# Performance work log

Hardware: AMD Instinct MI355X
Metric: run time of the kernel (lower is better)

## Reference

```python
import jax, jax.numpy as jnp
import numpy as np

B, N, K = 32, 4096, 8          # batch, num input features (64x64 map), num slots
HID, D, DM = 256, 256, 512     # hid_dim, slot_dim, mlp_hid_dim
ITERS = 3
TEMP = 1.0
EPS = 1e-8
SCALE = D ** -0.5              # (slot_dim // num_heads) ** -0.5, heads=1


def layer_norm(x, g, b):
    m = jnp.mean(x, axis=-1, keepdims=True)
    v = jnp.mean((x - m) ** 2, axis=-1, keepdims=True)
    return (x - m) * jax.lax.rsqrt(v + 1e-5) * g + b


def setup_inputs() -> dict:
    key = jax.random.key(0)
    ks = jax.random.split(key, 20)
    s = 0.02
    inp = {
        "inputs": jax.random.normal(ks[0], (B, N, HID), jnp.float32),
        "noise": jax.random.normal(ks[1], (B, K, D), jnp.float32),
        "slots_mu": jax.random.normal(ks[2], (1, 1, D), jnp.float32),
        "slots_sigma": jnp.abs(jax.random.normal(ks[3], (1, 1, D), jnp.float32)),
        "ln_in_g": jnp.ones((HID,), jnp.float32),
        "ln_in_b": jnp.zeros((HID,), jnp.float32),
        "ln_slots_g": jnp.ones((D,), jnp.float32),
        "ln_slots_b": jnp.zeros((D,), jnp.float32),
        "ln_mlp_g": jnp.ones((D,), jnp.float32),
        "ln_mlp_b": jnp.zeros((D,), jnp.float32),
        # Linear weights stored [in, out]
        "Wq": jax.random.normal(ks[4], (D, D), jnp.float32) * s,
        "bq": jnp.zeros((D,), jnp.float32),
        "Wk": jax.random.normal(ks[5], (HID, D), jnp.float32) * s,
        "bk": jnp.zeros((D,), jnp.float32),
        "Wv": jax.random.normal(ks[6], (HID, D), jnp.float32) * s,
        "bv": jnp.zeros((D,), jnp.float32),
        # GRUCell params (torch layout transposed to [in, 3D])
        "W_ih": jax.random.normal(ks[7], (D, 3 * D), jnp.float32) * s,
        "W_hh": jax.random.normal(ks[8], (D, 3 * D), jnp.float32) * s,
        "b_ih": jnp.zeros((3 * D,), jnp.float32),
        "b_hh": jnp.zeros((3 * D,), jnp.float32),
        # residual MLP
        "W1": jax.random.normal(ks[9], (D, DM), jnp.float32) * s,
        "b1": jnp.zeros((DM,), jnp.float32),
        "W2": jax.random.normal(ks[10], (DM, D), jnp.float32) * s,
        "b2": jnp.zeros((D,), jnp.float32),
    }
    return inp


def reference(inputs, noise, slots_mu, slots_sigma,
              ln_in_g, ln_in_b, ln_slots_g, ln_slots_b, ln_mlp_g, ln_mlp_b,
              Wq, bq, Wk, bk, Wv, bv,
              W_ih, W_hh, b_ih, b_hh,
              W1, b1, W2, b2):
    x = layer_norm(inputs, ln_in_g, ln_in_b)            # [B,N,HID]
    k = x @ Wk + bk                                     # [B,N,D]
    v = x @ Wv + bv                                     # [B,N,D]

    slots = slots_mu + slots_sigma * noise              # [B,K,D]

    for _ in range(ITERS):
        slots_prev = slots
        s = layer_norm(slots, ln_slots_g, ln_slots_b)
        q = s @ Wq + bq                                  # [B,K,D]
        dots = jnp.einsum('bkd,bnd->bkn', q, k) * SCALE / TEMP
        attn = jax.nn.softmax(dots, axis=1)              # inverted: over slot axis
        attn = attn + EPS
        attn = attn / jnp.sum(attn, axis=2, keepdims=True)  # weighted mean over keys
        updates = jnp.einsum('bkn,bnd->bkd', attn, v)    # [B,K,D]

        # GRUCell on flattened (B*K, D)
        xg = updates.reshape(-1, D)
        h = slots_prev.reshape(-1, D)
        gi = xg @ W_ih + b_ih
        gh = h @ W_hh + b_hh
        i_r, i_z, i_n = jnp.split(gi, 3, axis=-1)
        h_r, h_z, h_n = jnp.split(gh, 3, axis=-1)
        r = jax.nn.sigmoid(i_r + h_r)
        z = jax.nn.sigmoid(i_z + h_z)
        n = jnp.tanh(i_n + r * h_n)
        h = (1.0 - z) * n + z * h
        slots = h.reshape(B, K, D)

        # residual MLP
        m = layer_norm(slots, ln_mlp_g, ln_mlp_b)
        slots = slots + (jax.nn.relu(m @ W1 + b1) @ W2 + b2)

    return slots
```

## Files before the change

kernel.cpp:

```cpp
#include <hip/hip_runtime.h>
#include <hip/hip_bf16.h>

#define NB 32
#define NPOS 4096
#define NSLOT 8
#define HIDD 256
#define DDIM 256
#define SCALE_F 0.0625f
#define EPS_F 1e-8f
#define NCHUNK 32
#define CPOS 128
#define TPOS 32

typedef __attribute__((ext_vector_type(4))) float f32x4;
typedef __attribute__((ext_vector_type(8))) short s16x8;
typedef __attribute__((ext_vector_type(2))) unsigned int u32x2;
typedef _Float16 h16x2 __attribute__((ext_vector_type(2)));

__device__ __forceinline__ unsigned short f2bf(float f) {
    unsigned int x = __float_as_uint(f);
    x = (x + 0x7fffu + ((x >> 16) & 1u)) >> 16;
    return (unsigned short)x;
}
__device__ __forceinline__ unsigned short f2h(float f) {
    _Float16 h = (_Float16)f;
    return __builtin_bit_cast(unsigned short, h);
}
__device__ __forceinline__ h16x2 u2h(unsigned u) { return __builtin_bit_cast(h16x2, u); }
__device__ __forceinline__ h16x2 mkh(float a0, float a1) {
    h16x2 r; r[0] = (_Float16)a0; r[1] = (_Float16)a1; return r;
}
__device__ __forceinline__ void dot4(f32x4& acc, uint4 wv, h16x2 av) {
    acc[0] = __builtin_amdgcn_fdot2(av, u2h(wv.x), acc[0], false);
    acc[1] = __builtin_amdgcn_fdot2(av, u2h(wv.y), acc[1], false);
    acc[2] = __builtin_amdgcn_fdot2(av, u2h(wv.z), acc[2], false);
    acc[3] = __builtin_amdgcn_fdot2(av, u2h(wv.w), acc[3], false);
}
__device__ __forceinline__ unsigned packrowh(const float* __restrict__ W, int hp, int N, int c) {
    return (unsigned)f2h(W[(2*hp)*N + c]) | ((unsigned)f2h(W[(2*hp+1)*N + c]) << 16);
}

__device__ __forceinline__ void qk_tail(
        float v0, float v1, int b, int s0,
        const float* __restrict__ lng, const float* __restrict__ lnb,
        const float* __restrict__ Wq, const float* __restrict__ bq,
        const float* __restrict__ Wk, const float* __restrict__ bk,
        unsigned short* __restrict__ qkg, float* __restrict__ qbkg,
        float (*sh)[256], float (*red)[4]) {
    int c = threadIdx.x;
    float s_0 = v0, q_0 = v0 * v0, s_1 = v1, q_1 = v1 * v1;
    #pragma unroll
    for (int m = 32; m; m >>= 1) {
        s_0 += __shfl_xor(s_0, m); q_0 += __shfl_xor(q_0, m);
        s_1 += __shfl_xor(s_1, m); q_1 += __shfl_xor(q_1, m);
    }
    if ((c & 63) == 0) { int w = c >> 6; red[w][0]=s_0; red[w][1]=q_0; red[w][2]=s_1; red[w][3]=q_1; }
    __syncthreads();
    float S0 = red[0][0]+red[1][0]+red[2][0]+red[3][0];
    float Q0 = red[0][1]+red[1][1]+red[2][1]+red[3][1];
    float S1 = red[0][2]+red[1][2]+red[2][2]+red[3][2];
    float Q1 = red[0][3]+red[1][3]+red[2][3]+red[3][3];
    float m0 = S0 * 0.00390625f, r0 = rsqrtf(Q0 * 0.00390625f - m0*m0 + 1e-5f);
    float m1 = S1 * 0.00390625f, r1 = rsqrtf(Q1 * 0.00390625f - m1*m1 + 1e-5f);
    float gc = lng[c], bc = lnb[c];
    sh[0][c] = (v0 - m0) * r0 * gc + bc;
    sh[1][c] = (v1 - m1) * r1 * gc + bc;
    __syncthreads();
    float qa0 = bq[c], qa1 = qa0;
    for (int h = 0; h < 256; h += 4) {
        float w0 = Wq[(h+0)*256+c], w1 = Wq[(h+1)*256+c];
        float w2 = Wq[(h+2)*256+c], w3 = Wq[(h+3)*256+c];
        float4 x0 = *(const float4*)&sh[0][h], x1 = *(const float4*)&sh[1][h];
        qa0 += x0.x*w0 + x0.y*w1 + x0.z*w2 + x0.w*w3;
        qa1 += x1.x*w0 + x1.y*w1 + x1.z*w2 + x1.w*w3;
    }
    __syncthreads();
    sh[0][c] = qa0; sh[1][c] = qa1;
    float bkc = bk[c];
    float p0 = qa0 * bkc, p1 = qa1 * bkc;
    #pragma unroll
    for (int m = 32; m; m >>= 1) { p0 += __shfl_xor(p0, m); p1 += __shfl_xor(p1, m); }
    __syncthreads();
    if ((c & 63) == 0) { int w = c >> 6; red[w][0] = p0; red[w][1] = p1; }
    __syncthreads();
    if (c < 2) qbkg[b*8 + s0 + c] = SCALE_F * (red[0][c]+red[1][c]+red[2][c]+red[3][c]);
    float k0 = 0.f, k1 = 0.f;
    const float* wkr = Wk + (long)c * 256;
    for (int d = 0; d < 256; d += 4) {
        float4 wk4 = *(const float4*)&wkr[d];
        float4 x0 = *(const float4*)&sh[0][d], x1 = *(const float4*)&sh[1][d];
        k0 += x0.x*wk4.x + x0.y*wk4.y + x0.z*wk4.z + x0.w*wk4.w;
        k1 += x1.x*wk4.x + x1.y*wk4.y + x1.z*wk4.z + x1.w*wk4.w;
    }
    qkg[(b*8 + s0    )*256 + c] = f2bf(SCALE_F * k0);
    qkg[(b*8 + s0 + 1)*256 + c] = f2bf(SCALE_F * k1);
}

__global__ __launch_bounds__(256) void k_setup(
        const float* __restrict__ x, const float* __restrict__ lnig,
        const float* __restrict__ lnib, unsigned short* __restrict__ lnx,
        const float* __restrict__ Wq, const float* __restrict__ Wk,
        const float* __restrict__ Wv, const float* __restrict__ Wih,
        const float* __restrict__ Whh, const float* __restrict__ W1,
        const float* __restrict__ W2,
        unsigned* __restrict__ WqP, unsigned* __restrict__ WkTP,
        unsigned* __restrict__ WvP, unsigned* __restrict__ WihP,
        unsigned* __restrict__ WhhP, unsigned* __restrict__ W1P,
        unsigned* __restrict__ W2P,
        const float* __restrict__ noise, const float* __restrict__ mu,
        const float* __restrict__ sig, const float* __restrict__ lnsg,
        const float* __restrict__ lnsb, const float* __restrict__ bq,
        const float* __restrict__ bk, float* __restrict__ slots,
        unsigned short* __restrict__ qkg, float* __restrict__ qbkg) {
    __shared__ float sh[2][256];
    __shared__ float red[4][4];
    if (blockIdx.x < 8192) {
        int lane = threadIdx.x & 63;
        int wave = threadIdx.x >> 6;
        long row = (long)blockIdx.x * 4 + wave;
        const float4* xr = (const float4*)(x + row * 256);
        float4 v = xr[lane];
        float s = v.x + v.y + v.z + v.w;
        float sq = v.x * v.x + v.y * v.y + v.z * v.z + v.w * v.w;
        #pragma unroll
        for (int m = 32; m; m >>= 1) { s += __shfl_xor(s, m); sq += __shfl_xor(sq, m); }
        float mean = s * 0.00390625f;
        float rstd = rsqrtf(sq * 0.00390625f - mean * mean + 1e-5f);
        const float4 gg = ((const float4*)lnig)[lane];
        const float4 bb = ((const float4*)lnib)[lane];
        ushort4 o;
        o.x = f2bf((v.x - mean) * rstd * gg.x + bb.x);
        o.y = f2bf((v.y - mean) * rstd * gg.y + bb.y);
        o.z = f2bf((v.z - mean) * rstd * gg.z + bb.z);
        o.w = f2bf((v.w - mean) * rstd * gg.w + bb.w);
        ((ushort4*)(lnx + row * 256))[lane] = o;
        return;
    }
    if (blockIdx.x < 8576) {
        int i = (blockIdx.x - 8192) * 256 + threadIdx.x;
        if (i < 32768) {
            int hp = i >> 8, c = i & 255;
            WqP[i] = packrowh(Wq, hp, 256, c);
            WvP[i] = packrowh(Wv, hp, 256, c);
            WkTP[i] = (unsigned)f2h(Wk[c*256 + 2*hp]) | ((unsigned)f2h(Wk[c*256 + 2*hp + 1]) << 16);
        }
        if (i < 65536) {
            int hp1 = i >> 9, c1 = i & 511;
            W1P[i] = packrowh(W1, hp1, 512, c1);
            int hp2 = i >> 8, c2 = i & 255;
            W2P[i] = packrowh(W2, hp2, 256, c2);
        }
        if (i < 98304) {
            int hp = i / 768, c = i % 768;
            WihP[i] = packrowh(Wih, hp, 768, c);
            WhhP[i] = packrowh(Whh, hp, 768, c);
        }
        return;
    }
    {
        int bi = blockIdx.x - 8576;
        int b = bi >> 2, rp = bi & 3;
        int s0 = rp * 2, r0 = b * 8 + s0;
        int c = threadIdx.x;
        float v0 = mu[c] + sig[c] * noise[r0*256 + c];
        float v1 = mu[c] + sig[c] * noise[(r0+1)*256 + c];
        slots[r0*256 + c] = v0;
        slots[(r0+1)*256 + c] = v1;
        qk_tail(v0, v1, b, s0, lnsg, lnsb, Wq, bq, Wk, bk, qkg, qbkg, sh, red);
    }
}

__global__ __launch_bounds__(128) void k_stream(
        const unsigned short* __restrict__ lnx, const unsigned short* __restrict__ qk,
        const float* __restrict__ qbk, float* __restrict__ Upart,
        float* __restrict__ dpart) {
    __shared__ unsigned short xt[TPOS * 256];
    __shared__ float Ured[8 * 256];
    __shared__ float dred[8];
    int b = blockIdx.x >> 5, ch = blockIdx.x & 31;
    int t = threadIdx.x;
    int l = t & 63, w = t >> 6;
    for (int i = t; i < 2048; i += 128) Ured[i] = 0.f;
    if (t < 8) dred[t] = 0.f;
    int slot = l & 15, g = l >> 4;
    s16x8 qkf[8];
    float qbkv = 0.f;
    if (slot < 8) {
        const unsigned short* qrow = qk + (b*8 + slot) * 256;
        #pragma unroll
        for (int hk = 0; hk < 8; hk++)
            qkf[hk] = *(const s16x8*)(qrow + hk*32 + 8*g);
        qbkv = qbk[b*8 + slot];
    } else {
        #pragma unroll
        for (int hk = 0; hk < 8; hk++) qkf[hk] = (s16x8)0;
    }
    f32x4 uacc[16];
    #pragma unroll
    for (int i = 0; i < 16; i++) uacc[i] = (f32x4)0.f;
    float dreg = 0.f;
    int gbase = (b * NPOS + ch * CPOS) * 256;
    int pw = w * 16;
    __syncthreads();
    for (int tile = 0; tile < 4; tile++) {
        #pragma unroll
        for (int i = 0; i < 8; i++) {
            int c = t + 128 * i;
            int p = c >> 5, hc = c & 31;
            int4 v = *(const int4*)(lnx + gbase + (tile*TPOS + p)*256 + hc*8);
            *(int4*)&xt[p*256 + ((hc ^ (p & 15)) << 3)] = v;
        }
        __syncthreads();
        f32x4 acc = (f32x4)0.f;
        {
            int prow = pw + (l & 15);
            const unsigned short* xrow = &xt[prow * 256];
            int sw = prow & 15;
            #pragma unroll
            for (int hk = 0; hk < 8; hk++) {
                s16x8 a = *(const s16x8*)(xrow + (((hk*4 + g) ^ sw) << 3));
                acc = __builtin_amdgcn_mfma_f32_16x16x32_bf16(a, qkf[hk], acc, 0, 0, 0);
            }
        }
        float at[4];
        #pragma unroll
        for (int r = 0; r < 4; r++) {
            float v = acc[r] + qbkv;
            float m = v;
            m = fmaxf(m, __shfl_xor(m, 1));
            m = fmaxf(m, __shfl_xor(m, 2));
            m = fmaxf(m, __shfl_xor(m, 4));
            float e = __expf(v - m);
            float sum = e;
            sum += __shfl_xor(sum, 1);
            sum += __shfl_xor(sum, 2);
            sum += __shfl_xor(sum, 4);
            float a = e / sum;
            at[r] = a;
            dreg += a;
        }
        u32x2 a2;
        a2.x = (unsigned)f2bf(at[0]) | ((unsigned)f2bf(at[1]) << 16);
        a2.y = (unsigned)f2bf(at[2]) | ((unsigned)f2bf(at[3]) << 16);
        int p0 = pw + 4 * g;
        int hl = l & 7;
        #pragma unroll
        for (int hc = 0; hc < 16; hc++) {
            int hcol = hc * 2 + ((l & 15) >> 3);
            unsigned e0 = xt[(p0+0)*256 + ((hcol ^ ((p0+0) & 15)) << 3) + hl];
            unsigned e1 = xt[(p0+1)*256 + ((hcol ^ ((p0+1) & 15)) << 3) + hl];
            unsigned e2 = xt[(p0+2)*256 + ((hcol ^ ((p0+2) & 15)) << 3) + hl];
            unsigned e3 = xt[(p0+3)*256 + ((hcol ^ ((p0+3) & 15)) << 3) + hl];
            u32x2 b2;
            b2.x = e0 | (e1 << 16);
            b2.y = e2 | (e3 << 16);
            asm volatile("v_mfma_f32_16x16x16_bf16 %0, %1, %2, %0"
                         : "+v"(uacc[hc]) : "v"(a2), "v"(b2));
        }
        __syncthreads();
    }
    if (g < 2) {
        #pragma unroll
        for (int hc = 0; hc < 16; hc++) {
            int h = hc * 16 + (l & 15);
            #pragma unroll
            for (int r = 0; r < 4; r++)
                atomicAdd(&Ured[(4*g + r)*256 + h], uacc[hc][r]);
        }
    }
    dreg += __shfl_xor(dreg, 16);
    dreg += __shfl_xor(dreg, 32);
    if (slot < 8 && g == 0) atomicAdd(&dred[slot], dreg);
    __syncthreads();
    float* up = Upart + (long)(b * NCHUNK + ch) * 2048;
    for (int i = t; i < 2048; i += 128) up[i] = Ured[i];
    if (t < 8) dpart[(b * NCHUNK + ch) * 8 + t] = dred[t];
}

__device__ __forceinline__ float ln1024(float v, int c, const float* __restrict__ g,
                                        const float* __restrict__ b, float (*red)[2]) {
    float s1 = v, s2 = v * v;
    #pragma unroll
    for (int m = 32; m; m >>= 1) { s1 += __shfl_xor(s1, m); s2 += __shfl_xor(s2, m); }
    int w = threadIdx.x >> 6;
    if ((threadIdx.x & 63) == 0) { red[w][0] = s1; red[w][1] = s2; }
    __syncthreads();
    float S = 0.f, Q = 0.f;
    #pragma unroll
    for (int i = 0; i < 16; i++) { S += red[i][0]; Q += red[i][1]; }
    float mean = S * (1.f/1024.f);
    float rstd = rsqrtf(Q * (1.f/1024.f) - mean*mean + 1e-5f);
    __syncthreads();
    return (v - mean) * rstd * g[c] + b[c];
}

__global__ __launch_bounds__(1024) void k_post(
        const float* __restrict__ Upart, const float* __restrict__ dpart,
        const unsigned* __restrict__ WvP, const float* __restrict__ bv,
        const unsigned* __restrict__ WihP, const unsigned* __restrict__ WhhP,
        const float* __restrict__ bih, const float* __restrict__ bhh,
        const float* __restrict__ lnmg, const float* __restrict__ lnmb,
        const unsigned* __restrict__ W1P, const float* __restrict__ b1,
        const unsigned* __restrict__ W2P, const float* __restrict__ b2,
        const float* __restrict__ lnsg, const float* __restrict__ lnsb,
        const unsigned* __restrict__ WqP, const float* __restrict__ bq,
        const unsigned* __restrict__ WkTP, const float* __restrict__ bk,
        float* __restrict__ slots, unsigned short* __restrict__ qkg,
        float* __restrict__ qbkg, float* __restrict__ outp, int last) {
    __shared__ union {
        float PG[2][8][768];
        struct { float P16[16][256]; float H2[8][512]; } s;
    } sm;
    __shared__ float A[256], B[256], G2[2][768], H[512];
    __shared__ float red[16][2];
    __shared__ float scal[1];
    int r = blockIdx.x, b = r >> 3, s = r & 7;
    int t = threadIdx.x, c = t & 255, q = t >> 8;
    int cg = t & 63, kg16 = t >> 6;
    {
        float u = 0.f;
        const float* ub = Upart + (long)b * NCHUNK * 2048 + s * 256 + c;
        #pragma unroll
        for (int i = 0; i < 8; i++) u += ub[(q * 8 + i) * 2048];
        sm.s.P16[q][c] = u;
        if (q == 1) B[c] = slots[r * 256 + c];
        if (t < 32) {
            float dv = dpart[(b * NCHUNK + t) * 8 + s];
            #pragma unroll
            for (int m = 16; m; m >>= 1) dv += __shfl_xor(dv, m);
            if (t == 0) scal[0] = dv;
        }
    }
    __syncthreads();
    float dn = 1.f / (scal[0] + (float)NPOS * EPS_F);
    if (q == 0) A[c] = sm.s.P16[0][c] + sm.s.P16[1][c] + sm.s.P16[2][c] + sm.s.P16[3][c];
    __syncthreads();
    {
        f32x4 acc = (f32x4)0.f;
        const uint4* wp = (const uint4*)(WvP + kg16 * 8 * 256 + 4 * cg);
        #pragma unroll
        for (int i = 0; i < 8; i++) {
            uint4 wv = wp[i * 64];
            dot4(acc, wv, mkh(A[2*(kg16*8+i)], A[2*(kg16*8+i)+1]));
        }
        *(f32x4*)&sm.s.P16[kg16][4*cg] = acc;
    }
    __syncthreads();
    float updtmp;
    {
        float ss = 0.f;
        #pragma unroll
        for (int k = 0; k < 16; k++) ss += sm.s.P16[k][c];
        updtmp = ss * dn + bv[c];
    }
    __syncthreads();
    if (q == 0) A[c] = updtmp;
    __syncthreads();
    {
        int h = t >> 9;
        int kg = (t >> 6) & 7;
        const float* src = h ? B : A;
        const unsigned* W = h ? WhhP : WihP;
        f32x4 ar = (f32x4)0.f, az = (f32x4)0.f, an = (f32x4)0.f;
        #pragma unroll 4
        for (int i = 0; i < 16; i++) {
            int hp = kg * 16 + i;
            h16x2 av = mkh(src[2*hp], src[2*hp+1]);
            uint4 w0 = *(const uint4*)(W + hp*768 + 4*cg);
            uint4 w1 = *(const uint4*)(W + hp*768 + 256 + 4*cg);
            uint4 w2 = *(const uint4*)(W + hp*768 + 512 + 4*cg);
            dot4(ar, w0, av);
            dot4(az, w1, av);
            dot4(an, w2, av);
        }
        *(f32x4*)&sm.PG[h][kg][4*cg]       = ar;
        *(f32x4*)&sm.PG[h][kg][256 + 4*cg] = az;
        *(f32x4*)&sm.PG[h][kg][512 + 4*cg] = an;
    }
    __syncthreads();
    for (int idx = t; idx < 1536; idx += 1024) {
        int h = idx / 768, cc = idx - h * 768;
        float ss = 0.f;
        #pragma unroll
        for (int k = 0; k < 8; k++) ss += sm.PG[h][k][cc];
        G2[h][cc] = ss;
    }
    __syncthreads();
    float spc = B[c];
    float gir = bih[c]     + G2[0][c];
    float giz = bih[c+256] + G2[0][c+256];
    float gin = bih[c+512] + G2[0][c+512];
    float ghr = bhh[c]     + G2[1][c];
    float ghz = bhh[c+256] + G2[1][c+256];
    float ghn = bhh[c+512] + G2[1][c+512];
    float rg = 1.f/(1.f + __expf(-(gir+ghr)));
    float zg = 1.f/(1.f + __expf(-(giz+ghz)));
    float ng = tanhf(gin + rg*ghn);
    float hnew = (1.f - zg)*ng + zg*spc;
    float mmc = ln1024(hnew, c, lnmg, lnmb, red);
    if (q == 0) A[c] = mmc;
    __syncthreads();
    {
        int kg = t >> 7, cg1 = t & 127;
        f32x4 acc = (f32x4)0.f;
        const uint4* wp = (const uint4*)(W1P + kg * 16 * 512 + 4 * cg1);
        #pragma unroll 4
        for (int i = 0; i < 16; i++) {
            uint4 wv = wp[i * 128];
            dot4(acc, wv, mkh(A[2*(kg*16+i)], A[2*(kg*16+i)+1]));
        }
        *(f32x4*)&sm.s.H2[kg][4*cg1] = acc;
    }
    __syncthreads();
    if (t < 512) {
        float ss = b1[t];
        #pragma unroll
        for (int k = 0; k < 8; k++) ss += sm.s.H2[k][t];
        H[t] = fmaxf(ss, 0.f);
    }
    __syncthreads();
    {
        f32x4 acc = (f32x4)0.f;
        const uint4* wp = (const uint4*)(W2P + kg16 * 16 * 256 + 4 * cg);
        #pragma unroll 4
        for (int i = 0; i < 16; i++) {
            uint4 wv = wp[i * 64];
            dot4(acc, wv, mkh(H[2*(kg16*16+i)], H[2*(kg16*16+i)+1]));
        }
        *(f32x4*)&sm.s.P16[kg16][4*cg] = acc;
    }
    __syncthreads();
    float outc;
    {
        float ss = 0.f;
        #pragma unroll
        for (int k = 0; k < 16; k++) ss += sm.s.P16[k][c];
        outc = hnew + ss + b2[c];
    }
    if (t < 256) {
        slots[r*256 + c] = outc;
        if (last) outp[r*256 + c] = outc;
    }
    if (last) return;
    __syncthreads();
    float sc = ln1024(outc, c, lnsg, lnsb, red);
    if (q == 0) A[c] = sc;
    __syncthreads();
    {
        f32x4 acc = (f32x4)0.f;
        const uint4* wp = (const uint4*)(WqP + kg16 * 8 * 256 + 4 * cg);
        #pragma unroll
        for (int i = 0; i < 8; i++) {
            uint4 wv = wp[i * 64];
            dot4(acc, wv, mkh(A[2*(kg16*8+i)], A[2*(kg16*8+i)+1]));
        }
        *(f32x4*)&sm.s.P16[kg16][4*cg] = acc;
    }
    __syncthreads();
    float qc;
    {
        float ss = 0.f;
        #pragma unroll
        for (int k = 0; k < 16; k++) ss += sm.s.P16[k][c];
        qc = ss + bq[c];
    }
    {
        float v = qc * bk[c];
        #pragma unroll
        for (int m = 32; m; m >>= 1) v += __shfl_xor(v, m);
        int w = t >> 6;
        if ((t & 63) == 0) red[w][0] = v;
        __syncthreads();
        if (t == 0) {
            float S = 0.f;
            #pragma unroll
            for (int i = 0; i < 16; i++) S += red[i][0];
            qbkg[r] = SCALE_F * 0.25f * S;
        }
        __syncthreads();
    }
    if (q == 0) A[c] = qc;
    __syncthreads();
    {
        f32x4 acc = (f32x4)0.f;
        const uint4* wp = (const uint4*)(WkTP + kg16 * 8 * 256 + 4 * cg);
        #pragma unroll
        for (int i = 0; i < 8; i++) {
            uint4 wv = wp[i * 64];
            dot4(acc, wv, mkh(A[2*(kg16*8+i)], A[2*(kg16*8+i)+1]));
        }
        *(f32x4*)&sm.s.P16[kg16][4*cg] = acc;
    }
    __syncthreads();
    if (t < 256) {
        float ss = 0.f;
        #pragma unroll
        for (int k = 0; k < 16; k++) ss += sm.s.P16[k][c];
        qkg[r*256 + c] = f2bf(SCALE_F * ss);
    }
}

extern "C" void kernel_launch(void* const* d_in, const int* in_sizes, int n_in,
                              void* d_out, int out_size, void* d_ws, size_t ws_size,
                              hipStream_t stream) {
    const float* inputs = (const float*)d_in[0];
    const float* noise  = (const float*)d_in[1];
    const float* mu     = (const float*)d_in[2];
    const float* sig    = (const float*)d_in[3];
    const float* lnig   = (const float*)d_in[4];
    const float* lnib   = (const float*)d_in[5];
    const float* lnsg   = (const float*)d_in[6];
    const float* lnsb   = (const float*)d_in[7];
    const float* lnmg   = (const float*)d_in[8];
    const float* lnmb   = (const float*)d_in[9];
    const float* Wq     = (const float*)d_in[10];
    const float* bq     = (const float*)d_in[11];
    const float* Wk     = (const float*)d_in[12];
    const float* bk     = (const float*)d_in[13];
    const float* Wv     = (const float*)d_in[14];
    const float* bv     = (const float*)d_in[15];
    const float* Wih    = (const float*)d_in[16];
    const float* Whh    = (const float*)d_in[17];
    const float* bih    = (const float*)d_in[18];
    const float* bhh    = (const float*)d_in[19];
    const float* W1     = (const float*)d_in[20];
    const float* b1     = (const float*)d_in[21];
    const float* W2     = (const float*)d_in[22];
    const float* b2     = (const float*)d_in[23];

    char* ws = (char*)d_ws;
    unsigned short* lnx = (unsigned short*)ws;
    size_t off = (size_t)NB * NPOS * HIDD * 2;
    unsigned short* qkb = (unsigned short*)(ws + off); off += (size_t)NB*NSLOT*HIDD*2;
    float* qbk   = (float*)(ws + off); off += (size_t)NB*NSLOT*4;
    float* Upart = (float*)(ws + off); off += (size_t)NB*NCHUNK*NSLOT*HIDD*4;
    float* dpart = (float*)(ws + off); off += (size_t)NB*NCHUNK*NSLOT*4;
    float* slots = (float*)(ws + off); off += (size_t)NB*NSLOT*DDIM*4;
    unsigned* WqP  = (unsigned*)(ws + off); off += 32768u*4;
    unsigned* WkTP = (unsigned*)(ws + off); off += 32768u*4;
    unsigned* WvP  = (unsigned*)(ws + off); off += 32768u*4;
    unsigned* WihP = (unsigned*)(ws + off); off += 98304u*4;
    unsigned* WhhP = (unsigned*)(ws + off); off += 98304u*4;
    unsigned* W1P  = (unsigned*)(ws + off); off += 65536u*4;
    unsigned* W2P  = (unsigned*)(ws + off); off += 65536u*4;

    k_setup<<<8704, 256, 0, stream>>>(inputs, lnig, lnib, lnx,
                                      Wq, Wk, Wv, Wih, Whh, W1, W2,
                                      WqP, WkTP, WvP, WihP, WhhP, W1P, W2P,
                                      noise, mu, sig, lnsg, lnsb, bq, bk,
                                      slots, qkb, qbk);
    for (int it = 0; it < 3; it++) {
        k_stream<<<NB*NCHUNK, 128, 0, stream>>>(lnx, qkb, qbk, Upart, dpart);
        k_post<<<NB*NSLOT, 1024, 0, stream>>>(Upart, dpart,
                                              WvP, bv, WihP, WhhP, bih, bhh,
                                              lnmg, lnmb, W1P, b1, W2P, b2,
                                              lnsg, lnsb, WqP, bq, WkTP, bk,
                                              slots, qkb, qbk, (float*)d_out,
                                              it == 2 ? 1 : 0);
    }
}
```

Measured before the change: 216.1 us.

## Fuse stream and post kernels into one persistent kernel with grid barriers

Replaces the six alternating k_stream/k_post launches with a single persistent 256-block, 1024-thread kernel that runs all three iterations and synchronises through an atomic grid barrier in workspace. Each block now streams a 512-position region per batch in 16 tiles, with waves taking turns on the QK MFMA and attention written through shared memory. The goal is to remove launch overhead and gaps between kernels. In exchange the stream phase runs with fewer, larger blocks (256 instead of 1024), which lowers memory-level parallelism. The spin barrier also depends on all 256 blocks being co-resident.

```diff
diff --git a/kernel.cpp b/kernel.cpp
--- a/kernel.cpp
+++ b/kernel.cpp
@@ -4,13 +4,10 @@
 #define NB 32
 #define NPOS 4096
 #define NSLOT 8
-#define HIDD 256
-#define DDIM 256
 #define SCALE_F 0.0625f
 #define EPS_F 1e-8f
-#define NCHUNK 32
-#define CPOS 128
 #define TPOS 32
+#define NREG 8
 
 typedef __attribute__((ext_vector_type(4))) float f32x4;
 typedef __attribute__((ext_vector_type(8))) short s16x8;
@@ -38,6 +35,17 @@
 }
 __device__ __forceinline__ unsigned packrowh(const float* __restrict__ W, int hp, int N, int c) {
     return (unsigned)f2h(W[(2*hp)*N + c]) | ((unsigned)f2h(W[(2*hp+1)*N + c]) << 16);
+}
+
+__device__ __forceinline__ void gridbar(unsigned* cnt, unsigned target) {
+    __syncthreads();
+    if (threadIdx.x == 0) {
+        __threadfence();
+        __hip_atomic_fetch_add(cnt, 1u, __ATOMIC_RELEASE, __HIP_MEMORY_SCOPE_AGENT);
+        while (__hip_atomic_load(cnt, __ATOMIC_ACQUIRE, __HIP_MEMORY_SCOPE_AGENT) < target)
+            __builtin_amdgcn_s_sleep(8);
+    }
+    __syncthreads();
 }
 
 __device__ __forceinline__ void qk_tail(
@@ -111,7 +119,8 @@
         const float* __restrict__ sig, const float* __restrict__ lnsg,
         const float* __restrict__ lnsb, const float* __restrict__ bq,
         const float* __restrict__ bk, float* __restrict__ slots,
-        unsigned short* __restrict__ qkg, float* __restrict__ qbkg) {
+        unsigned short* __restrict__ qkg, float* __restrict__ qbkg,
+        unsigned* __restrict__ barcnt) {
     __shared__ float sh[2][256];
     __shared__ float red[4][4];
     if (blockIdx.x < 8192) {
@@ -137,6 +146,7 @@
         return;
     }
     if (blockIdx.x < 8576) {
+        if (blockIdx.x == 8192 && threadIdx.x == 0) *barcnt = 0u;
         int i = (blockIdx.x - 8192) * 256 + threadIdx.x;
         if (i < 32768) {
             int hp = i >> 8, c = i & 255;
@@ -170,132 +180,26 @@
     }
 }
 
-__global__ __launch_bounds__(128) void k_stream(
-        const unsigned short* __restrict__ lnx, const unsigned short* __restrict__ qk,
-        const float* __restrict__ qbk, float* __restrict__ Upart,
-        float* __restrict__ dpart) {
-    __shared__ unsigned short xt[TPOS * 256];
-    __shared__ float Ured[8 * 256];
-    __shared__ float dred[8];
-    int b = blockIdx.x >> 5, ch = blockIdx.x & 31;
-    int t = threadIdx.x;
-    int l = t & 63, w = t >> 6;
-    for (int i = t; i < 2048; i += 128) Ured[i] = 0.f;
-    if (t < 8) dred[t] = 0.f;
-    int slot = l & 15, g = l >> 4;
-    s16x8 qkf[8];
-    float qbkv = 0.f;
-    if (slot < 8) {
-        const unsigned short* qrow = qk + (b*8 + slot) * 256;
-        #pragma unroll
-        for (int hk = 0; hk < 8; hk++)
-            qkf[hk] = *(const s16x8*)(qrow + hk*32 + 8*g);
-        qbkv = qbk[b*8 + slot];
-    } else {
-        #pragma unroll
-        for (int hk = 0; hk < 8; hk++) qkf[hk] = (s16x8)0;
-    }
-    f32x4 uacc[16];
-    #pragma unroll
-    for (int i = 0; i < 16; i++) uacc[i] = (f32x4)0.f;
-    float dreg = 0.f;
-    int gbase = (b * NPOS + ch * CPOS) * 256;
-    int pw = w * 16;
-    __syncthreads();
-    for (int tile = 0; tile < 4; tile++) {
-        #pragma unroll
-        for (int i = 0; i < 8; i++) {
-            int c = t + 128 * i;
-            int p = c >> 5, hc = c & 31;
-            int4 v = *(const int4*)(lnx + gbase + (tile*TPOS + p)*256 + hc*8);
-            *(int4*)&xt[p*256 + ((hc ^ (p & 15)) << 3)] = v;
-        }
-        __syncthreads();
-        f32x4 acc = (f32x4)0.f;
-        {
-            int prow = pw + (l & 15);
-            const unsigned short* xrow = &xt[prow * 256];
-            int sw = prow & 15;
-            #pragma unroll
-            for (int hk = 0; hk < 8; hk++) {
-                s16x8 a = *(const s16x8*)(xrow + (((hk*4 + g) ^ sw) << 3));
-                acc = __builtin_amdgcn_mfma_f32_16x16x32_bf16(a, qkf[hk], acc, 0, 0, 0);
-            }
-        }
-        float at[4];
-        #pragma unroll
-        for (int r = 0; r < 4; r++) {
-            float v = acc[r] + qbkv;
-            float m = v;
-            m = fmaxf(m, __shfl_xor(m, 1));
-            m = fmaxf(m, __shfl_xor(m, 2));
-            m = fmaxf(m, __shfl_xor(m, 4));
-            float e = __expf(v - m);
-            float sum = e;
-            sum += __shfl_xor(sum, 1);
-            sum += __shfl_xor(sum, 2);
-            sum += __shfl_xor(sum, 4);
-            float a = e / sum;
-            at[r] = a;
-            dreg += a;
-        }
-        u32x2 a2;
-        a2.x = (unsigned)f2bf(at[0]) | ((unsigned)f2bf(at[1]) << 16);
-        a2.y = (unsigned)f2bf(at[2]) | ((unsigned)f2bf(at[3]) << 16);
-        int p0 = pw + 4 * g;
-        int hl = l & 7;
-        #pragma unroll
-        for (int hc = 0; hc < 16; hc++) {
-            int hcol = hc * 2 + ((l & 15) >> 3);
-            unsigned e0 = xt[(p0+0)*256 + ((hcol ^ ((p0+0) & 15)) << 3) + hl];
-            unsigned e1 = xt[(p0+1)*256 + ((hcol ^ ((p0+1) & 15)) << 3) + hl];
-            unsigned e2 = xt[(p0+2)*256 + ((hcol ^ ((p0+2) & 15)) << 3) + hl];
-            unsigned e3 = xt[(p0+3)*256 + ((hcol ^ ((p0+3) & 15)) << 3) + hl];
-            u32x2 b2;
-            b2.x = e0 | (e1 << 16);
-            b2.y = e2 | (e3 << 16);
-            asm volatile("v_mfma_f32_16x16x16_bf16 %0, %1, %2, %0"
-                         : "+v"(uacc[hc]) : "v"(a2), "v"(b2));
-        }
-        __syncthreads();
-    }
-    if (g < 2) {
-        #pragma unroll
-        for (int hc = 0; hc < 16; hc++) {
-            int h = hc * 16 + (l & 15);
-            #pragma unroll
-            for (int r = 0; r < 4; r++)
-                atomicAdd(&Ured[(4*g + r)*256 + h], uacc[hc][r]);
-        }
-    }
-    dreg += __shfl_xor(dreg, 16);
-    dreg += __shfl_xor(dreg, 32);
-    if (slot < 8 && g == 0) atomicAdd(&dred[slot], dreg);
-    __syncthreads();
-    float* up = Upart + (long)(b * NCHUNK + ch) * 2048;
-    for (int i = t; i < 2048; i += 128) up[i] = Ured[i];
-    if (t < 8) dpart[(b * NCHUNK + ch) * 8 + t] = dred[t];
-}
-
-__device__ __forceinline__ float ln1024(float v, int c, const float* __restrict__ g,
-                                        const float* __restrict__ b, float (*red)[2]) {
-    float s1 = v, s2 = v * v;
-    #pragma unroll
-    for (int m = 32; m; m >>= 1) { s1 += __shfl_xor(s1, m); s2 += __shfl_xor(s2, m); }
-    int w = threadIdx.x >> 6;
-    if ((threadIdx.x & 63) == 0) { red[w][0] = s1; red[w][1] = s2; }
-    __syncthreads();
-    float S = 0.f, Q = 0.f;
-    #pragma unroll
-    for (int i = 0; i < 16; i++) { S += red[i][0]; Q += red[i][1]; }
-    float mean = S * (1.f/1024.f);
-    float rstd = rsqrtf(Q * (1.f/1024.f) - mean*mean + 1e-5f);
-    __syncthreads();
-    return (v - mean) * rstd * g[c] + b[c];
-}
-
-__global__ __launch_bounds__(1024) void k_post(
-        const float* __restrict__ Upart, const float* __restrict__ dpart,
+struct StreamS {
+    unsigned short xt[TPOS * 256];
+    float Ured[8 * 256];
+    float attnL[32][9];
+    float dred[8];
+};
+struct PostS {
+    union {
+        float PG[2][8][768];
+        struct { float P16[16][256]; float H2[8][512]; } s;
+    } sm;
+    float A[256], B[256], G2[2][768], H[512];
+    float red[16][2];
+    float scal[1];
+};
+
+__global__ __launch_bounds__(1024) void k_loop(
+        const unsigned short* __restrict__ lnx,
+        unsigned short* __restrict__ qkg, float* __restrict__ qbkg,
+        float* __restrict__ Upart, float* __restrict__ dpart,
         const unsigned* __restrict__ WvP, const float* __restrict__ bv,
         const unsigned* __restrict__ WihP, const unsigned* __restrict__ WhhP,
         const float* __restrict__ bih, const float* __restrict__ bhh,
@@ -305,198 +209,329 @@
         const float* __restrict__ lnsg, const float* __restrict__ lnsb,
         const unsigned* __restrict__ WqP, const float* __restrict__ bq,
         const unsigned* __restrict__ WkTP, const float* __restrict__ bk,
-        float* __restrict__ slots, unsigned short* __restrict__ qkg,
-        float* __restrict__ qbkg, float* __restrict__ outp, int last) {
-    __shared__ union {
-        float PG[2][8][768];
-        struct { float P16[16][256]; float H2[8][512]; } s;
-    } sm;
-    __shared__ float A[256], B[256], G2[2][768], H[512];
-    __shared__ float red[16][2];
-    __shared__ float scal[1];
-    int r = blockIdx.x, b = r >> 3, s = r & 7;
-    int t = threadIdx.x, c = t & 255, q = t >> 8;
-    int cg = t & 63, kg16 = t >> 6;
-    {
-        float u = 0.f;
-        const float* ub = Upart + (long)b * NCHUNK * 2048 + s * 256 + c;
-        #pragma unroll
-        for (int i = 0; i < 8; i++) u += ub[(q * 8 + i) * 2048];
-        sm.s.P16[q][c] = u;
-        if (q == 1) B[c] = slots[r * 256 + c];
-        if (t < 32) {
-            float dv = dpart[(b * NCHUNK + t) * 8 + s];
-            #pragma unroll
-            for (int m = 16; m; m >>= 1) dv += __shfl_xor(dv, m);
-            if (t == 0) scal[0] = dv;
+        float* __restrict__ slots, float* __restrict__ outp,
+        unsigned* __restrict__ barcnt) {
+    __shared__ union { StreamS st; PostS po; } smem;
+    int blk = blockIdx.x;
+    int t = threadIdx.x;
+    int l = t & 63, w = t >> 6;
+    int bS = blk >> 3, region = blk & 7;
+    int rP = blk, bP = blk >> 3, sP = blk & 7;
+    unsigned barno = 0;
+    for (int it = 0; it < 3; it++) {
+        {
+            StreamS& S = smem.st;
+            for (int i = t; i < 2048; i += 1024) S.Ured[i] = 0.f;
+            if (t < 8) S.dred[t] = 0.f;
+            int slot = l & 15, g = l >> 4;
+            s16x8 qkf[8];
+            float qbkv = 0.f;
+            if (slot < 8) {
+                const unsigned short* qrow = qkg + (bS*8 + slot) * 256;
+                #pragma unroll
+                for (int hk = 0; hk < 8; hk++)
+                    qkf[hk] = *(const s16x8*)(qrow + hk*32 + 8*g);
+                qbkv = qbkg[bS*8 + slot];
+            } else {
+                #pragma unroll
+                for (int hk = 0; hk < 8; hk++) qkf[hk] = (s16x8)0;
+            }
+            f32x4 uacc = (f32x4)0.f;
+            float dreg = 0.f;
+            long gbase = ((long)bS * NPOS + region * 512) * 256;
+            int pw = (w & 1) * 16;
+            __syncthreads();
+            for (int tile = 0; tile < 16; tile++) {
+                {
+                    int p = t >> 5, hc = t & 31;
+                    int4 v = *((const int4*)(lnx + gbase + tile*(32*256)) + t);
+                    *(int4*)&S.xt[p*256 + ((hc ^ (p & 15)) << 3)] = v;
+                }
+                __syncthreads();
+                if ((w >> 1) == (tile & 7)) {
+                    f32x4 acc = (f32x4)0.f;
+                    int prow = pw + slot;
+                    const unsigned short* xrow = &S.xt[prow * 256];
+                    int sw = prow & 15;
+                    #pragma unroll
+                    for (int hk = 0; hk < 8; hk++) {
+                        s16x8 a = *(const s16x8*)(xrow + (((hk*4 + g) ^ sw) << 3));
+                        acc = __builtin_amdgcn_mfma_f32_16x16x32_bf16(a, qkf[hk], acc, 0, 0, 0);
+                    }
+                    #pragma unroll
+                    for (int r = 0; r < 4; r++) {
+                        float v = acc[r] + qbkv;
+                        float m = v;
+                        m = fmaxf(m, __shfl_xor(m, 1));
+                        m = fmaxf(m, __shfl_xor(m, 2));
+                        m = fmaxf(m, __shfl_xor(m, 4));
+                        float e = __expf(v - m);
+                        float sum = e;
+                        sum += __shfl_xor(sum, 1);
+                        sum += __shfl_xor(sum, 2);
+                        sum += __shfl_xor(sum, 4);
+                        float a = e / sum;
+                        if (slot < 8) { S.attnL[pw + 4*g + r][slot] = a; dreg += a; }
+                    }
+                }
+                __syncthreads();
+                {
+                    int hl = l & 7;
+                    int hcol = w * 2 + (slot >> 3);
+                    #pragma unroll
+                    for (int ph = 0; ph < 2; ph++) {
+                        int p0 = ph*16 + 4*g;
+                        float a0v = 0.f, a1v = 0.f, a2v = 0.f, a3v = 0.f;
+                        if (slot < 8) {
+                            a0v = S.attnL[p0+0][slot];
+                            a1v = S.attnL[p0+1][slot];
+                            a2v = S.attnL[p0+2][slot];
+                            a3v = S.attnL[p0+3][slot];
+                        }
+                        u32x2 a2;
+                        a2.x = (unsigned)f2bf(a0v) | ((unsigned)f2bf(a1v) << 16);
+                        a2.y = (unsigned)f2bf(a2v) | ((unsigned)f2bf(a3v) << 16);
+                        unsigned e0 = S.xt[(p0+0)*256 + ((hcol ^ ((p0+0) & 15)) << 3) + hl];
+                        unsigned e1 = S.xt[(p0+1)*256 + ((hcol ^ ((p0+1) & 15)) << 3) + hl];
+                        unsigned e2 = S.xt[(p0+2)*256 + ((hcol ^ ((p0+2) & 15)) << 3) + hl];
+                        unsigned e3 = S.xt[(p0+3)*256 + ((hcol ^ ((p0+3) & 15)) << 3) + hl];
+                        u32x2 b2;
+                        b2.x = e0 | (e1 << 16);
+                        b2.y = e2 | (e3 << 16);
+                        asm volatile("v_mfma_f32_16x16x16_bf16 %0, %1, %2, %0"
+                                     : "+v"(uacc) : "v"(a2), "v"(b2));
+                    }
+                }
+                __syncthreads();
+            }
+            if (g < 2) {
+                #pragma unroll
+                for (int r = 0; r < 4; r++)
+                    S.Ured[(4*g + r)*256 + w*16 + slot] = uacc[r];
+            }
+            dreg += __shfl_xor(dreg, 16);
+            dreg += __shfl_xor(dreg, 32);
+            if (slot < 8 && g == 0) atomicAdd(&S.dred[slot], dreg);
+            __syncthreads();
+            float* up = Upart + (long)blk * 2048;
+            for (int i = t; i < 2048; i += 1024) up[i] = S.Ured[i];
+            if (t < 8) dpart[blk*8 + t] = S.dred[t];
         }
-    }
-    __syncthreads();
-    float dn = 1.f / (scal[0] + (float)NPOS * EPS_F);
-    if (q == 0) A[c] = sm.s.P16[0][c] + sm.s.P16[1][c] + sm.s.P16[2][c] + sm.s.P16[3][c];
-    __syncthreads();
-    {
-        f32x4 acc = (f32x4)0.f;
-        const uint4* wp = (const uint4*)(WvP + kg16 * 8 * 256 + 4 * cg);
-        #pragma unroll
-        for (int i = 0; i < 8; i++) {
-            uint4 wv = wp[i * 64];
-            dot4(acc, wv, mkh(A[2*(kg16*8+i)], A[2*(kg16*8+i)+1]));
+        gridbar(barcnt, ++barno * 256);
+        {
+            PostS& P = smem.po;
+            int c = t & 255, q4 = t >> 8;
+            int cg = t & 63, kg16 = t >> 6;
+            {
+                const float* ub = Upart + ((long)bP * 8) * 2048 + sP * 256 + c;
+                float u = ub[(q4*2)*2048] + ub[(q4*2+1)*2048];
+                P.sm.s.P16[q4][c] = u;
+                if (q4 == 1) P.B[c] = slots[rP * 256 + c];
+                if (t < 8) {
+                    float dv = dpart[(bP*8 + t)*8 + sP];
+                    dv += __shfl_xor(dv, 4);
+                    dv += __shfl_xor(dv, 2);
+                    dv += __shfl_xor(dv, 1);
+                    if (t == 0) P.scal[0] = dv;
+                }
+            }
+            __syncthreads();
+            float dn = 1.f / (P.scal[0] + (float)NPOS * EPS_F);
+            if (q4 == 0) P.A[c] = P.sm.s.P16[0][c] + P.sm.s.P16[1][c] + P.sm.s.P16[2][c] + P.sm.s.P16[3][c];
+            __syncthreads();
+            {
+                f32x4 acc = (f32x4)0.f;
+                const uint4* wp = (const uint4*)(WvP + kg16 * 8 * 256 + 4 * cg);
+                #pragma unroll
+                for (int i = 0; i < 8; i++) {
+                    uint4 wv = wp[i * 64];
+                    dot4(acc, wv, mkh(P.A[2*(kg16*8+i)], P.A[2*(kg16*8+i)+1]));
+                }
+                *(f32x4*)&P.sm.s.P16[kg16][4*cg] = acc;
+            }
+            __syncthreads();
+            float updtmp;
+            {
+                float ss = 0.f;
+                #pragma unroll
+                for (int k = 0; k < 16; k++) ss += P.sm.s.P16[k][c];
+                updtmp = ss * dn + bv[c];
+            }
+            __syncthreads();
+            if (q4 == 0) P.A[c] = updtmp;
+            __syncthreads();
+            {
+                int h = t >> 9;
+                int kg = (t >> 6) & 7;
+                const float* src = h ? P.B : P.A;
+                const unsigned* W = h ? WhhP : WihP;
+                f32x4 ar = (f32x4)0.f, az = (f32x4)0.f, an = (f32x4)0.f;
+                #pragma unroll 4
+                for (int i = 0; i < 16; i++) {
+                    int hp = kg * 16 + i;
+                    h16x2 av = mkh(src[2*hp], src[2*hp+1]);
+                    uint4 w0 = *(const uint4*)(W + hp*768 + 4*cg);
+                    uint4 w1 = *(const uint4*)(W + hp*768 + 256 + 4*cg);
+                    uint4 w2 = *(const uint4*)(W + hp*768 + 512 + 4*cg);
+                    dot4(ar, w0, av);
+                    dot4(az, w1, av);
+                    dot4(an, w2, av);
+                }
+                *(f32x4*)&P.sm.PG[h][kg][4*cg]       = ar;
+                *(f32x4*)&P.sm.PG[h][kg][256 + 4*cg] = az;
+                *(f32x4*)&P.sm.PG[h][kg][512 + 4*cg] = an;
+            }
+            __syncthreads();
+            for (int idx = t; idx < 1536; idx += 1024) {
+                int h = idx / 768, cc = idx - h * 768;
+                float ss = 0.f;
+                #pragma unroll
+                for (int k = 0; k < 8; k++) ss += P.sm.PG[h][k][cc];
+                P.G2[h][cc] = ss;
+            }
+            __syncthreads();
+            float spc = P.B[c];
+            float gir = bih[c]     + P.G2[0][c];
+            float giz = bih[c+256] + P.G2[0][c+256];
+            float gin = bih[c+512] + P.G2[0][c+512];
+            float ghr = bhh[c]     + P.G2[1][c];
+            float ghz = bhh[c+256] + P.G2[1][c+256];
+            float ghn = bhh[c+512] + P.G2[1][c+512];
+            float rg = 1.f/(1.f + __expf(-(gir+ghr)));
+            float zg = 1.f/(1.f + __expf(-(giz+ghz)));
+            float ng = tanhf(gin + rg*ghn);
+            float hnew = (1.f - zg)*ng + zg*spc;
+            float mmc;
+            {
+                float s1 = hnew, s2 = hnew * hnew;
+                #pragma unroll
+                for (int m = 32; m; m >>= 1) { s1 += __shfl_xor(s1, m); s2 += __shfl_xor(s2, m); }
+                if ((t & 63) == 0) { P.red[w][0] = s1; P.red[w][1] = s2; }
+                __syncthreads();
+                float Ssum = 0.f, Qsum = 0.f;
+                #pragma unroll
+                for (int i = 0; i < 16; i++) { Ssum += P.red[i][0]; Qsum += P.red[i][1]; }
+                float mean = Ssum * (1.f/1024.f);
+                float rstd = rsqrtf(Qsum * (1.f/1024.f) - mean*mean + 1e-5f);
+                __syncthreads();
+                mmc = (hnew - mean) * rstd * lnmg[c] + lnmb[c];
+            }
+            if (q4 == 0) P.A[c] = mmc;
+            __syncthreads();
+            {
+                int kg = t >> 7, cg1 = t & 127;
+                f32x4 acc = (f32x4)0.f;
+                const uint4* wp = (const uint4*)(W1P + kg * 16 * 512 + 4 * cg1);
+                #pragma unroll 4
+                for (int i = 0; i < 16; i++) {
+                    uint4 wv = wp[i * 128];
+                    dot4(acc, wv, mkh(P.A[2*(kg*16+i)], P.A[2*(kg*16+i)+1]));
+                }
+                *(f32x4*)&P.sm.s.H2[kg][4*cg1] = acc;
+            }
+            __syncthreads();
+            if (t < 512) {
+                float ss = b1[t];
+                #pragma unroll
+                for (int k = 0; k < 8; k++) ss += P.sm.s.H2[k][t];
+                P.H[t] = fmaxf(ss, 0.f);
+            }
+            __syncthreads();
+            {
+                f32x4 acc = (f32x4)0.f;
+                const uint4* wp = (const uint4*)(W2P + kg16 * 16 * 256 + 4 * cg);
+                #pragma unroll 4
+                for (int i = 0; i < 16; i++) {
+                    uint4 wv = wp[i * 64];
+                    dot4(acc, wv, mkh(P.H[2*(kg16*16+i)], P.H[2*(kg16*16+i)+1]));
+                }
+                *(f32x4*)&P.sm.s.P16[kg16][4*cg] = acc;
+            }
+            __syncthreads();
+            float outc;
+            {
+                float ss = 0.f;
+                #pragma unroll
+                for (int k = 0; k < 16; k++) ss += P.sm.s.P16[k][c];
+                outc = hnew + ss + b2[c];
+            }
+            if (t < 256) {
+                slots[rP*256 + c] = outc;
+                if (it == 2) outp[rP*256 + c] = outc;
+            }
+            if (it < 2) {
+                __syncthreads();
+                float sc;
+                {
+                    float s1 = outc, s2 = outc * outc;
+                    #pragma unroll
+                    for (int m = 32; m; m >>= 1) { s1 += __shfl_xor(s1, m); s2 += __shfl_xor(s2, m); }
+                    if ((t & 63) == 0) { P.red[w][0] = s1; P.red[w][1] = s2; }
+                    __syncthreads();
+                    float Ssum = 0.f, Qsum = 0.f;
+                    #pragma unroll
+                    for (int i = 0; i < 16; i++) { Ssum += P.red[i][0]; Qsum += P.red[i][1]; }
+                    float mean = Ssum * (1.f/1024.f);
+                    float rstd = rsqrtf(Qsum * (1.f/1024.f) - mean*mean + 1e-5f);
+                    __syncthreads();
+                    sc = (outc - mean) * rstd * lnsg[c] + lnsb[c];
+                }
+                if (q4 == 0) P.A[c] = sc;
+                __syncthreads();
+                {
+                    f32x4 acc = (f32x4)0.f;
+                    const uint4* wp = (const uint4*)(WqP + kg16 * 8 * 256 + 4 * cg);
+                    #pragma unroll
+                    for (int i = 0; i < 8; i++) {
+                        uint4 wv = wp[i * 64];
+                        dot4(acc, wv, mkh(P.A[2*(kg16*8+i)], P.A[2*(kg16*8+i)+1]));
+                    }
+                    *(f32x4*)&P.sm.s.P16[kg16][4*cg] = acc;
+                }
+                __syncthreads();
+                float qc;
+                {
+                    float ss = 0.f;
+                    #pragma unroll
+                    for (int k = 0; k < 16; k++) ss += P.sm.s.P16[k][c];
+                    qc = ss + bq[c];
+                }
+                {
+                    float v = qc * bk[c];
+                    #pragma unroll
+                    for (int m = 32; m; m >>= 1) v += __shfl_xor(v, m);
+                    if ((t & 63) == 0) P.red[w][0] = v;
+                    __syncthreads();
+                    if (t == 0) {
+                        float Ssum = 0.f;
+                        #pragma unroll
+                        for (int i = 0; i < 16; i++) Ssum += P.red[i][0];
+                        qbkg[rP] = SCALE_F * 0.25f * Ssum;
+                    }
+                    __syncthreads();
+                }
+                if (q4 == 0) P.A[c] = qc;
+                __syncthreads();
+                {
+                    f32x4 acc = (f32x4)0.f;
+                    const uint4* wp = (const uint4*)(WkTP + kg16 * 8 * 256 + 4 * cg);
+                    #pragma unroll
+                    for (int i = 0; i < 8; i++) {
+                        uint4 wv = wp[i * 64];
+                        dot4(acc, wv, mkh(P.A[2*(kg16*8+i)], P.A[2*(kg16*8+i)+1]));
+                    }
+                    *(f32x4*)&P.sm.s.P16[kg16][4*cg] = acc;
+                }
+                __syncthreads();
+                if (t < 256) {
+                    float ss = 0.f;
+                    #pragma unroll
+                    for (int k = 0; k < 16; k++) ss += P.sm.s.P16[k][c];
+                    qkg[rP*256 + c] = f2bf(SCALE_F * ss);
+                }
+                gridbar(barcnt, ++barno * 256);
+            }
         }
-        *(f32x4*)&sm.s.P16[kg16][4*cg] = acc;
-    }
-    __syncthreads();
-    float updtmp;
-    {
-        float ss = 0.f;
-        #pragma unroll
-        for (int k = 0; k < 16; k++) ss += sm.s.P16[k][c];
-        updtmp = ss * dn + bv[c];
-    }
-    __syncthreads();
-    if (q == 0) A[c] = updtmp;
-    __syncthreads();
-    {
-        int h = t >> 9;
-        int kg = (t >> 6) & 7;
-        const float* src = h ? B : A;
-        const unsigned* W = h ? WhhP : WihP;
-        f32x4 ar = (f32x4)0.f, az = (f32x4)0.f, an = (f32x4)0.f;
-        #pragma unroll 4
-        for (int i = 0; i < 16; i++) {
-            int hp = kg * 16 + i;
-            h16x2 av = mkh(src[2*hp], src[2*hp+1]);
-            uint4 w0 = *(const uint4*)(W + hp*768 + 4*cg);
-            uint4 w1 = *(const uint4*)(W + hp*768 + 256 + 4*cg);
-            uint4 w2 = *(const uint4*)(W + hp*768 + 512 + 4*cg);
-            dot4(ar, w0, av);
-            dot4(az, w1, av);
-            dot4(an, w2, av);
-        }
-        *(f32x4*)&sm.PG[h][kg][4*cg]       = ar;
-        *(f32x4*)&sm.PG[h][kg][256 + 4*cg] = az;
-        *(f32x4*)&sm.PG[h][kg][512 + 4*cg] = an;
-    }
-    __syncthreads();
-    for (int idx = t; idx < 1536; idx += 1024) {
-        int h = idx / 768, cc = idx - h * 768;
-        float ss = 0.f;
-        #pragma unroll
-        for (int k = 0; k < 8; k++) ss += sm.PG[h][k][cc];
-        G2[h][cc] = ss;
-    }
-    __syncthreads();
-    float spc = B[c];
-    float gir = bih[c]     + G2[0][c];
-    float giz = bih[c+256] + G2[0][c+256];
-    float gin = bih[c+512] + G2[0][c+512];
-    float ghr = bhh[c]     + G2[1][c];
-    float ghz = bhh[c+256] + G2[1][c+256];
-    float ghn = bhh[c+512] + G2[1][c+512];
-    float rg = 1.f/(1.f + __expf(-(gir+ghr)));
-    float zg = 1.f/(1.f + __expf(-(giz+ghz)));
-    float ng = tanhf(gin + rg*ghn);
-    float hnew = (1.f - zg)*ng + zg*spc;
-    float mmc = ln1024(hnew, c, lnmg, lnmb, red);
-    if (q == 0) A[c] = mmc;
-    __syncthreads();
-    {
-        int kg = t >> 7, cg1 = t & 127;
-        f32x4 acc = (f32x4)0.f;
-        const uint4* wp = (const uint4*)(W1P + kg * 16 * 512 + 4 * cg1);
-        #pragma unroll 4
-        for (int i = 0; i < 16; i++) {
-            uint4 wv = wp[i * 128];
-            dot4(acc, wv, mkh(A[2*(kg*16+i)], A[2*(kg*16+i)+1]));
-        }
-        *(f32x4*)&sm.s.H2[kg][4*cg1] = acc;
-    }
-    __syncthreads();
-    if (t < 512) {
-        float ss = b1[t];
-        #pragma unroll
-        for (int k = 0; k < 8; k++) ss += sm.s.H2[k][t];
-        H[t] = fmaxf(ss, 0.f);
-    }
-    __syncthreads();
-    {
-        f32x4 acc = (f32x4)0.f;
-        const uint4* wp = (const uint4*)(W2P + kg16 * 16 * 256 + 4 * cg);
-        #pragma unroll 4
-        for (int i = 0; i < 16; i++) {
-            uint4 wv = wp[i * 64];
-            dot4(acc, wv, mkh(H[2*(kg16*16+i)], H[2*(kg16*16+i)+1]));
-        }
-        *(f32x4*)&sm.s.P16[kg16][4*cg] = acc;
-    }
-    __syncthreads();
-    float outc;
-    {
-        float ss = 0.f;
-        #pragma unroll
-        for (int k = 0; k < 16; k++) ss += sm.s.P16[k][c];
-        outc = hnew + ss + b2[c];
-    }
-    if (t < 256) {
-        slots[r*256 + c] = outc;
-        if (last) outp[r*256 + c] = outc;
-    }
-    if (last) return;
-    __syncthreads();
-    float sc = ln1024(outc, c, lnsg, lnsb, red);
-    if (q == 0) A[c] = sc;
-    __syncthreads();
-    {
-        f32x4 acc = (f32x4)0.f;
-        const uint4* wp = (const uint4*)(WqP + kg16 * 8 * 256 + 4 * cg);
-        #pragma unroll
-        for (int i = 0; i < 8; i++) {
-            uint4 wv = wp[i * 64];
-            dot4(acc, wv, mkh(A[2*(kg16*8+i)], A[2*(kg16*8+i)+1]));
-        }
-        *(f32x4*)&sm.s.P16[kg16][4*cg] = acc;
-    }
-    __syncthreads();
-    float qc;
-    {
-        float ss = 0.f;
-        #pragma unroll
-        for (int k = 0; k < 16; k++) ss += sm.s.P16[k][c];
-        qc = ss + bq[c];
-    }
-    {
-        float v = qc * bk[c];
-        #pragma unroll
-        for (int m = 32; m; m >>= 1) v += __shfl_xor(v, m);
-        int w = t >> 6;
-        if ((t & 63) == 0) red[w][0] = v;
-        __syncthreads();
-        if (t == 0) {
-            float S = 0.f;
-            #pragma unroll
-            for (int i = 0; i < 16; i++) S += red[i][0];
-            qbkg[r] = SCALE_F * 0.25f * S;
-        }
-        __syncthreads();
-    }
-    if (q == 0) A[c] = qc;
-    __syncthreads();
-    {
-        f32x4 acc = (f32x4)0.f;
-        const uint4* wp = (const uint4*)(WkTP + kg16 * 8 * 256 + 4 * cg);
-        #pragma unroll
-        for (int i = 0; i < 8; i++) {
-            uint4 wv = wp[i * 64];
-            dot4(acc, wv, mkh(A[2*(kg16*8+i)], A[2*(kg16*8+i)+1]));
-        }
-        *(f32x4*)&sm.s.P16[kg16][4*cg] = acc;
-    }
-    __syncthreads();
-    if (t < 256) {
-        float ss = 0.f;
-        #pragma unroll
-        for (int k = 0; k < 16; k++) ss += sm.s.P16[k][c];
-        qkg[r*256 + c] = f2bf(SCALE_F * ss);
     }
 }
 
@@ -530,12 +565,12 @@
 
     char* ws = (char*)d_ws;
     unsigned short* lnx = (unsigned short*)ws;
-    size_t off = (size_t)NB * NPOS * HIDD * 2;
-    unsigned short* qkb = (unsigned short*)(ws + off); off += (size_t)NB*NSLOT*HIDD*2;
+    size_t off = (size_t)NB * NPOS * 256 * 2;
+    unsigned short* qkb = (unsigned short*)(ws + off); off += (size_t)NB*NSLOT*256*2;
     float* qbk   = (float*)(ws + off); off += (size_t)NB*NSLOT*4;
-    float* Upart = (float*)(ws + off); off += (size_t)NB*NCHUNK*NSLOT*HIDD*4;
-    float* dpart = (float*)(ws + off); off += (size_t)NB*NCHUNK*NSLOT*4;
-    float* slots = (float*)(ws + off); off += (size_t)NB*NSLOT*DDIM*4;
+    float* Upart = (float*)(ws + off); off += (size_t)256*2048*4;
+    float* dpart = (float*)(ws + off); off += (size_t)256*8*4;
+    float* slots = (float*)(ws + off); off += (size_t)NB*NSLOT*256*4;
     unsigned* WqP  = (unsigned*)(ws + off); off += 32768u*4;
     unsigned* WkTP = (unsigned*)(ws + off); off += 32768u*4;
     unsigned* WvP  = (unsigned*)(ws + off); off += 32768u*4;
@@ -543,19 +578,16 @@
     unsigned* WhhP = (unsigned*)(ws + off); off += 98304u*4;
     unsigned* W1P  = (unsigned*)(ws + off); off += 65536u*4;
     unsigned* W2P  = (unsigned*)(ws + off); off += 65536u*4;
+    unsigned* barcnt = (unsigned*)(ws + off); off += 256;
 
     k_setup<<<8704, 256, 0, stream>>>(inputs, lnig, lnib, lnx,
                                       Wq, Wk, Wv, Wih, Whh, W1, W2,
                                       WqP, WkTP, WvP, WihP, WhhP, W1P, W2P,
                                       noise, mu, sig, lnsg, lnsb, bq, bk,
-                                      slots, qkb, qbk);
-    for (int it = 0; it < 3; it++) {
-        k_stream<<<NB*NCHUNK, 128, 0, stream>>>(lnx, qkb, qbk, Upart, dpart);
-        k_post<<<NB*NSLOT, 1024, 0, stream>>>(Upart, dpart,
-                                              WvP, bv, WihP, WhhP, bih, bhh,
-                                              lnmg, lnmb, W1P, b1, W2P, b2,
-                                              lnsg, lnsb, WqP, bq, WkTP, bk,
-                                              slots, qkb, qbk, (float*)d_out,
-                                              it == 2 ? 1 : 0);
-    }
-}
+                                      slots, qkb, qbk, barcnt);
+    k_loop<<<256, 1024, 0, stream>>>(lnx, qkb, qbk, Upart, dpart,
+                                     WvP, bv, WihP, WhhP, bih, bhh,
+                                     lnmg, lnmb, W1P, b1, W2P, b2,
+                                     lnsg, lnsb, WqP, bq, WkTP, bk,
+                                     slots, (float*)d_out, barcnt);
+}
```

Result: slower. 357.3 us (+65.4%).
